# Optimization experiments

Measured on AMD Instinct MI355X. Metric: run time of the kernel, lower is better.

Reference implementation:

```python
import jax, jax.numpy as jnp
import numpy as np

N = 50000   # nodes
E = 800000  # edges
F = 128     # feat_dim
LN_EPS = 1e-5


def setup_inputs() -> dict:
    key = jax.random.key(0)
    ks = jax.random.split(key, 16)

    def lin(k, fan_in, shape):
        # roughly kaiming-uniform-like scale; exact init is irrelevant for correctness
        return jax.random.normal(k, shape, jnp.float32) * (1.0 / np.sqrt(fan_in))

    inp = {
        "x": jax.random.normal(ks[0], (N, F), jnp.float32),
        "pos": jax.random.normal(ks[1], (N, 3), jnp.float32),
        "edge_index": jax.random.randint(ks[2], (2, E), 0, N, jnp.int64),
        # edge_mlp: Linear(2F+1 -> F), SiLU, Linear(F -> F)
        "ew1": lin(ks[3], 2 * F + 1, (2 * F + 1, F)),
        "eb1": jnp.zeros((F,), jnp.float32),
        "ew2": lin(ks[4], F, (F, F)),
        "eb2": jnp.zeros((F,), jnp.float32),
        # node_mlp: Linear(F -> F), SiLU, Linear(F -> F)
        "nw1": lin(ks[5], F, (F, F)),
        "nb1": jnp.zeros((F,), jnp.float32),
        "nw2": lin(ks[6], F, (F, F)),
        "nb2": jnp.zeros((F,), jnp.float32),
        # coord_mlp: Linear(F -> 1), Tanh
        "cw": lin(ks[7], F, (F, 1)),
        "cb": jnp.zeros((1,), jnp.float32),
        # LayerNorm(F)
        "gamma": jnp.ones((F,), jnp.float32),
        "beta": jnp.zeros((F,), jnp.float32),
    }
    return inp


def reference(x, pos, edge_index, ew1, eb1, ew2, eb2, nw1, nb1, nw2, nb2, cw, cb, gamma, beta):
    row, col = edge_index[0], edge_index[1]

    diff = pos[row] - pos[col]                              # [E, 3]
    dist2 = jnp.sum(diff * diff, axis=1, keepdims=True)     # [E, 1]
    edge_feat = jnp.concatenate([x[row], x[col], dist2], axis=1)  # [E, 2F+1]

    # edge MLP (dropout p=0 -> identity in eval)
    msg = jax.nn.silu(edge_feat @ ew1 + eb1) @ ew2 + eb2    # [E, F]

    # scatter-add messages to source nodes
    agg = jax.ops.segment_sum(msg, row, num_segments=N)     # [N, F]

    # node MLP + residual + LayerNorm
    upd = jax.nn.silu(agg @ nw1 + nb1) @ nw2 + nb2          # [N, F]
    pre = x + upd
    mean = jnp.mean(pre, axis=-1, keepdims=True)
    var = jnp.mean(jnp.square(pre - mean), axis=-1, keepdims=True)
    x_out = gamma * (pre - mean) * jax.lax.rsqrt(var + LN_EPS) + beta

    # coordinate update
    scale = jnp.tanh(msg @ cw + cb)                         # [E, 1]
    delta = jax.ops.segment_sum(scale * diff, row, num_segments=N)  # [N, 3]
    pos_out = pos + delta
    return (x_out, pos_out)
```

## Files before the change

### kernel.cpp

```cpp
#include <hip/hip_runtime.h>
#include <math.h>

#define NN 50000
#define EE 800000
#define FF 128

constexpr float LN_EPS = 1e-5f;
constexpr int NC = (NN + 255) / 256;

typedef float  f32x4  __attribute__((ext_vector_type(4)));
typedef short  s16x8  __attribute__((ext_vector_type(8)));
typedef unsigned short u16x4 __attribute__((ext_vector_type(4)));

__device__ __forceinline__ float silu_f(float v) {
    return v / (1.f + __expf(-v));
}

__device__ __forceinline__ unsigned short f2bf(float f) {
    union { float f; unsigned u; } cv; cv.f = f;
    unsigned u = cv.u;
    u += 0x7fffu + ((u >> 16) & 1u);
    return (unsigned short)(u >> 16);
}

__device__ __forceinline__ float bf2f(unsigned short u) {
    union { unsigned u; float f; } cv; cv.u = ((unsigned)u) << 16;
    return cv.f;
}

constexpr int CVT_BLKS  = (NN * FF / 8) / 256;
constexpr int TRW_BLKS  = (32768 + 3 * 16384) / 256;
constexpr int HIST_BLKS = (EE + 255) / 256;

__global__ __launch_bounds__(256) void prep_kernel(
    const float* __restrict__ x, unsigned short* __restrict__ xb,
    const float* __restrict__ ew1, const float* __restrict__ ew2,
    const float* __restrict__ nw1, const float* __restrict__ nw2,
    unsigned short* __restrict__ ew1T, unsigned short* __restrict__ ew2T,
    unsigned short* __restrict__ nw1T, unsigned short* __restrict__ nw2T,
    const int* __restrict__ ei, int* __restrict__ cnt)
{
    if (blockIdx.x < CVT_BLKS) {
        int i = (blockIdx.x * 256 + threadIdx.x) * 8;
        float4 a = *(const float4*)&x[i];
        float4 b = *(const float4*)&x[i + 4];
        s16x8 o;
        o[0] = (short)f2bf(a.x); o[1] = (short)f2bf(a.y);
        o[2] = (short)f2bf(a.z); o[3] = (short)f2bf(a.w);
        o[4] = (short)f2bf(b.x); o[5] = (short)f2bf(b.y);
        o[6] = (short)f2bf(b.z); o[7] = (short)f2bf(b.w);
        *(s16x8*)&xb[i] = o;
    } else if (blockIdx.x < CVT_BLKS + TRW_BLKS) {
        int o = (blockIdx.x - CVT_BLKS) * 256 + threadIdx.x;
        if (o < 32768) {
            int n = o >> 8, k = o & 255;
            ew1T[o] = f2bf(ew1[k * FF + n]);
        } else if (o < 49152) {
            int o2 = o - 32768; int n = o2 >> 7, k = o2 & 127;
            ew2T[o2] = f2bf(ew2[k * FF + n]);
        } else if (o < 65536) {
            int o2 = o - 49152; int n = o2 >> 7, k = o2 & 127;
            nw1T[o2] = f2bf(nw1[k * FF + n]);
        } else {
            int o2 = o - 65536; int n = o2 >> 7, k = o2 & 127;
            nw2T[o2] = f2bf(nw2[k * FF + n]);
        }
    } else {
        int e = (blockIdx.x - CVT_BLKS - TRW_BLKS) * 256 + threadIdx.x;
        if (e < EE) atomicAdd(&cnt[ei[e]], 1);
    }
}

constexpr int YABS = 136;
constexpr int YNBLK = (NN + 63) / 64;

__global__ __launch_bounds__(512) void nodeY_kernel(
    const unsigned short* __restrict__ xb,
    const unsigned short* __restrict__ ew1T,
    unsigned short* __restrict__ Y)
{
    __shared__ __align__(16) unsigned short aB[64 * YABS];

    const int t   = threadIdx.x;
    const int w   = t >> 6;
    const int l   = t & 63;
    const int l15 = l & 15;
    const int q8  = l >> 4;
    const int n0  = blockIdx.x * 64;
    const int n   = w * 16 + l15;

    #pragma unroll
    for (int i = 0; i < 2; ++i) {
        int idx = (i * 512 + t) * 8;
        int e = idx >> 7, c = idx & 127;
        s16x8 v = {};
        if (n0 + e < NN) v = *(const s16x8*)(xb + (size_t)(n0 + e) * FF + c);
        *(s16x8*)(aB + e * YABS + c) = v;
    }
    __syncthreads();

    s16x8 ba[4], bb[4];
    #pragma unroll
    for (int ko = 0; ko < 4; ++ko) {
        ba[ko] = *(const s16x8*)(ew1T + (size_t)n * 256 + ko * 32 + q8 * 8);
        bb[ko] = *(const s16x8*)(ew1T + (size_t)n * 256 + 128 + ko * 32 + q8 * 8);
    }

    f32x4 acc1[4] = {}, acc2[4] = {};
    #pragma unroll
    for (int mt = 0; mt < 4; ++mt) {
        const unsigned short* ar = aB + (mt * 16 + l15) * YABS + q8 * 8;
        #pragma unroll
        for (int ko = 0; ko < 4; ++ko) {
            s16x8 a = *(const s16x8*)(ar + ko * 32);
            acc1[mt] = __builtin_amdgcn_mfma_f32_16x16x32_bf16(a, ba[ko], acc1[mt], 0, 0, 0);
            acc2[mt] = __builtin_amdgcn_mfma_f32_16x16x32_bf16(a, bb[ko], acc2[mt], 0, 0, 0);
        }
    }
    #pragma unroll
    for (int mt = 0; mt < 4; ++mt) {
        #pragma unroll
        for (int r = 0; r < 4; ++r) {
            int nn = n0 + mt * 16 + q8 * 4 + r;
            if (nn < NN) {
                Y[(size_t)nn * 256 + n]       = f2bf(acc1[mt][r]);
                Y[(size_t)nn * 256 + 128 + n] = f2bf(acc2[mt][r]);
            }
        }
    }
}

__global__ __launch_bounds__(256) void chunk_sum_kernel(
    const int* __restrict__ cnt, int* __restrict__ chunkSum)
{
    __shared__ int s[256];
    int t = threadIdx.x;
    int idx = blockIdx.x * 256 + t;
    s[t] = (idx < NN) ? cnt[idx] : 0;
    __syncthreads();
    for (int off = 128; off > 0; off >>= 1) {
        if (t < off) s[t] += s[t + off];
        __syncthreads();
    }
    if (t == 0) chunkSum[blockIdx.x] = s[0];
}

__global__ __launch_bounds__(256) void scan_chunks_kernel(
    const int* __restrict__ chunkSum, int* __restrict__ chunkOff)
{
    __shared__ int s[256];
    int t = threadIdx.x;
    int v = (t < NC) ? chunkSum[t] : 0;
    s[t] = v;
    __syncthreads();
    for (int off = 1; off < 256; off <<= 1) {
        int u = (t >= off) ? s[t - off] : 0;
        __syncthreads();
        s[t] += u;
        __syncthreads();
    }
    if (t < NC) chunkOff[t] = s[t] - v;
}

__global__ __launch_bounds__(256) void scan_kernel(
    const int* __restrict__ cnt, const int* __restrict__ chunkOff,
    int* __restrict__ offs, int* __restrict__ rowStart)
{
    __shared__ int s[256];
    int t = threadIdx.x;
    int idx = blockIdx.x * 256 + t;
    int v = (idx < NN) ? cnt[idx] : 0;
    s[t] = v;
    __syncthreads();
    for (int off = 1; off < 256; off <<= 1) {
        int u = (t >= off) ? s[t - off] : 0;
        __syncthreads();
        s[t] += u;
        __syncthreads();
    }
    if (idx < NN) {
        int st = chunkOff[blockIdx.x] + s[t] - v;
        offs[idx] = st;
        rowStart[idx] = st;
    }
}

__global__ __launch_bounds__(256) void scatter_idx_kernel(
    const int* __restrict__ ei, int* __restrict__ offs,
    int2* __restrict__ sPair)
{
    int e = blockIdx.x * 256 + threadIdx.x;
    if (e < EE) {
        int r = ei[e], c = ei[EE + e];
        int p = atomicAdd(&offs[r], 1);
        sPair[p] = make_int2(r, c);
    }
}

constexpr int EPB    = 64;
constexpr int NTILE  = EE / EPB;
constexpr int GRID_A = 2500;
constexpr int XAS    = 264;
constexpr int H1S    = 136;
constexpr int MTS    = 72;

__global__ __launch_bounds__(512, 4) void edgeA_kernel(
    const unsigned short* __restrict__ Yb, const float* __restrict__ pos,
    const int2* __restrict__ sPair,
    const float* __restrict__ ew1, const float* __restrict__ eb1,
    const unsigned short* __restrict__ ew2T, const float* __restrict__ eb2,
    const float* __restrict__ cw,  const float* __restrict__ cb,
    float* __restrict__ agg, float* __restrict__ sSg)
{
    __shared__ float dist2S[EPB];
    __shared__ int   rowS[2][EPB];
    __shared__ float sPartT[EPB][8];
    __shared__ __align__(16) unsigned short ya  [EPB * XAS];
    __shared__ __align__(16) unsigned short h1  [EPB * H1S];
    __shared__ __align__(16) unsigned short msgT[FF * MTS];

    const int t   = threadIdx.x;
    const int w   = t >> 6;
    const int l   = t & 63;
    const int l15 = l & 15;
    const int q8  = l >> 4;
    const int n   = w * 16 + l15;

    int swz;
    {
        const int qd = GRID_A >> 3, r8 = GRID_A & 7;
        int xcd = blockIdx.x & 7, p8 = blockIdx.x >> 3;
        swz = (xcd < r8 ? xcd * (qd + 1) : r8 * (qd + 1) + (xcd - r8) * qd) + p8;
    }

    s16x8 B2[4];
    #pragma unroll
    for (int ko = 0; ko < 4; ++ko)
        B2[ko] = *(const s16x8*)(ew2T + (size_t)n * 128 + ko * 32 + q8 * 8);
    const float b2   = eb2[n];
    const float cwc  = cw[n];
    const float cb0  = cb[0];

    const int c8 = (t & 15) * 8;
    const int e2 = (t >> 4) * 2;
    float w256r[8], b1r[8];
    {
        float4 wa = *(const float4*)&ew1[256 * FF + c8];
        float4 wb = *(const float4*)&ew1[256 * FF + c8 + 4];
        w256r[0]=wa.x; w256r[1]=wa.y; w256r[2]=wa.z; w256r[3]=wa.w;
        w256r[4]=wb.x; w256r[5]=wb.y; w256r[6]=wb.z; w256r[7]=wb.w;
        float4 ca = *(const float4*)&eb1[c8];
        float4 cbv = *(const float4*)&eb1[c8 + 4];
        b1r[0]=ca.x; b1r[1]=ca.y; b1r[2]=ca.z; b1r[3]=ca.w;
        b1r[4]=cbv.x; b1r[5]=cbv.y; b1r[6]=cbv.z; b1r[7]=cbv.w;
    }

    const int q    = t & 31;
    const int eB   = t >> 5;
    const int ksel = (q & 15) * 8;
    const bool useRow = (q < 16);
    const int colOff = useRow ? 0 : 128;

    int   nidx[4];
    s16x8 ag[4];
    {
        int e0 = swz * EPB;
        #pragma unroll
        for (int i = 0; i < 4; ++i) {
            int2 pr = sPair[e0 + eB + 16 * i];
            nidx[i] = useRow ? pr.x : pr.y;
        }
        #pragma unroll
        for (int i = 0; i < 4; ++i)
            ag[i] = *(const s16x8*)(Yb + (size_t)nidx[i] * 256 + colOff + ksel);
    }

    int bsel = 0;
    for (int tile = swz; tile < NTILE; tile += GRID_A) {
        const int e0 = tile * EPB;

        #pragma unroll
        for (int i = 0; i < 4; ++i)
            *(s16x8*)(ya + (eB + 16 * i) * XAS + q * 8) = ag[i];
        if (t < EPB) {
            int2 pr = sPair[e0 + t];
            int r = pr.x, c = pr.y;
            rowS[bsel][t] = r;
            float dx = pos[r*3+0] - pos[c*3+0];
            float dy = pos[r*3+1] - pos[c*3+1];
            float dz = pos[r*3+2] - pos[c*3+2];
            dist2S[t] = dx*dx + dy*dy + dz*dz;
        }
        __syncthreads();

        {
            int tn  = tile + GRID_A;
            int e0n = (tn < NTILE) ? tn * EPB : 0;
            #pragma unroll
            for (int i = 0; i < 4; ++i) {
                int2 pr = sPair[e0n + eB + 16 * i];
                nidx[i] = useRow ? pr.x : pr.y;
            }
            #pragma unroll
            for (int i = 0; i < 4; ++i)
                ag[i] = *(const s16x8*)(Yb + (size_t)nidx[i] * 256 + colOff + ksel);
        }

        #pragma unroll
        for (int s = 0; s < 2; ++s) {
            int e = e2 + s;
            s16x8 y1 = *(const s16x8*)(ya + e * XAS + c8);
            s16x8 y2 = *(const s16x8*)(ya + e * XAS + 128 + c8);
            float d2 = dist2S[e];
            s16x8 o;
            #pragma unroll
            for (int j = 0; j < 8; ++j) {
                float v = bf2f((unsigned short)y1[j]) + bf2f((unsigned short)y2[j])
                        + d2 * w256r[j] + b1r[j];
                o[j] = (short)f2bf(silu_f(v));
            }
            *(s16x8*)(h1 + e * H1S + c8) = o;
        }
        __syncthreads();

        f32x4 acc2[4] = {};
        #pragma unroll
        for (int mt = 0; mt < 4; ++mt) {
            const unsigned short* hr = h1 + (mt * 16 + l15) * H1S + q8 * 8;
            #pragma unroll
            for (int ko = 0; ko < 4; ++ko) {
                s16x8 a = *(const s16x8*)(hr + ko * 32);
                acc2[mt] = __builtin_amdgcn_mfma_f32_16x16x32_bf16(a, B2[ko], acc2[mt], 0, 0, 0);
            }
        }

        #pragma unroll
        for (int mt = 0; mt < 4; ++mt) {
            u16x4 o;
            #pragma unroll
            for (int r = 0; r < 4; ++r) {
                float m = acc2[mt][r] + b2;
                o[r] = f2bf(m);
                float p = m * cwc;
                p += __shfl_xor(p, 1);
                p += __shfl_xor(p, 2);
                p += __shfl_xor(p, 4);
                p += __shfl_xor(p, 8);
                if (l15 == 0) sPartT[mt * 16 + q8 * 4 + r][w] = p;
            }
            int b  = mt * 2 + (q8 >> 1);
            int bs = b ^ (n & 7);
            *(u16x4*)(msgT + n * MTS + bs * 8 + (q8 & 1) * 4) = o;
        }
        __syncthreads();

        {
            int e  = t >> 3;
            int ww = t & 7;
            float p = sPartT[e][ww];
            p += __shfl_xor(p, 1);
            p += __shfl_xor(p, 2);
            p += __shfl_xor(p, 4);
            if (ww == 0) sSg[e0 + e] = tanhf(p + cb0);
        }

        {
            int c    = t & 127;
            int s    = t >> 7;
            int base = s * 16;
            int b0 = (2 * s)     ^ (c & 7);
            int b1 = (2 * s + 1) ^ (c & 7);
            s16x8 v0 = *(const s16x8*)(msgT + c * MTS + b0 * 8);
            s16x8 v1 = *(const s16x8*)(msgT + c * MTS + b1 * 8);
            float a  = 0.f;
            int cur  = rowS[bsel][base];
            #pragma unroll
            for (int k = 0; k < 16; ++k) {
                int r = rowS[bsel][base + k];
                if (r != cur) {
                    atomicAdd(&agg[(size_t)cur * FF + c], a);
                    a = 0.f; cur = r;
                }
                unsigned short mv = (k < 8) ? (unsigned short)v0[k]
                                            : (unsigned short)v1[k - 8];
                a += bf2f(mv);
            }
            atomicAdd(&agg[(size_t)cur * FF + c], a);
        }
        bsel ^= 1;
    }
}

constexpr int NPB  = 64;
constexpr int ABS  = 136;
constexpr int NBLK = (NN + NPB - 1) / NPB;

__global__ __launch_bounds__(512) void nodeB_kernel(
    const float* __restrict__ x, const float* __restrict__ pos,
    const float* __restrict__ agg, const float* __restrict__ sSg,
    const int2* __restrict__ sPair, const int* __restrict__ rowStart,
    const unsigned short* __restrict__ nw1T, const float* __restrict__ nb1,
    const unsigned short* __restrict__ nw2T, const float* __restrict__ nb2,
    const float* __restrict__ gamma, const float* __restrict__ beta,
    float* __restrict__ xout, float* __restrict__ posout)
{
    __shared__ __align__(16) unsigned short aB [NPB * ABS];
    __shared__ __align__(16) unsigned short h1B[NPB * ABS];
    __shared__ float sRedS[8][NPB];
    __shared__ float sRedQ[8][NPB];

    const int t   = threadIdx.x;
    const int w   = t >> 6;
    const int l   = t & 63;
    const int l15 = l & 15;
    const int q8  = l >> 4;
    const int n0  = blockIdx.x * NPB;
    const int n   = w * 16 + l15;

    #pragma unroll
    for (int i = 0; i < 4; ++i) {
        int idx = (i * 512 + t) * 4;
        int e = idx >> 7, c = idx & 127;
        u16x4 o;
        if (n0 + e < NN) {
            float4 v = *(const float4*)&agg[(size_t)(n0 + e) * FF + c];
            o[0] = f2bf(v.x); o[1] = f2bf(v.y); o[2] = f2bf(v.z); o[3] = f2bf(v.w);
        } else {
            o[0] = 0; o[1] = 0; o[2] = 0; o[3] = 0;
        }
        *(u16x4*)(aB + e * ABS + c) = o;
    }

    {
        int e  = t >> 3;
        int ch = t & 7;
        int nn = n0 + e;
        bool ok = nn < NN;
        int p0 = ok ? rowStart[nn] : 0;
        int p1 = ok ? ((nn == NN - 1) ? EE : rowStart[nn + 1]) : 0;
        float px = ok ? pos[nn*3+0] : 0.f;
        float py = ok ? pos[nn*3+1] : 0.f;
        float pz = ok ? pos[nn*3+2] : 0.f;
        float sx = 0.f, sy = 0.f, sz = 0.f;
        for (int p = p0 + ch; p < p1; p += 8) {
            int c = sPair[p].y;
            float g = sSg[p];
            sx += g * (px - pos[c*3+0]);
            sy += g * (py - pos[c*3+1]);
            sz += g * (pz - pos[c*3+2]);
        }
        #pragma unroll
        for (int off = 1; off < 8; off <<= 1) {
            sx += __shfl_xor(sx, off);
            sy += __shfl_xor(sy, off);
            sz += __shfl_xor(sz, off);
        }
        if (ch == 0 && ok) {
            posout[nn*3+0] = px + sx;
            posout[nn*3+1] = py + sy;
            posout[nn*3+2] = pz + sz;
        }
    }
    __syncthreads();

    f32x4 acc[4] = {};
    {
        s16x8 bw[4];
        #pragma unroll
        for (int ko = 0; ko < 4; ++ko)
            bw[ko] = *(const s16x8*)(nw1T + (size_t)n * 128 + ko * 32 + q8 * 8);
        #pragma unroll
        for (int mt = 0; mt < 4; ++mt) {
            const unsigned short* ar = aB + (mt * 16 + l15) * ABS + q8 * 8;
            #pragma unroll
            for (int ko = 0; ko < 4; ++ko) {
                s16x8 a = *(const s16x8*)(ar + ko * 32);
                acc[mt] = __builtin_amdgcn_mfma_f32_16x16x32_bf16(a, bw[ko], acc[mt], 0, 0, 0);
            }
        }
    }
    {
        float bb = nb1[n];
        #pragma unroll
        for (int mt = 0; mt < 4; ++mt) {
            #pragma unroll
            for (int r = 0; r < 4; ++r) {
                int e = mt * 16 + q8 * 4 + r;
                h1B[e * ABS + n] = f2bf(silu_f(acc[mt][r] + bb));
            }
        }
    }
    __syncthreads();

    f32x4 acc2[4] = {};
    {
        s16x8 bw[4];
        #pragma unroll
        for (int ko = 0; ko < 4; ++ko)
            bw[ko] = *(const s16x8*)(nw2T + (size_t)n * 128 + ko * 32 + q8 * 8);
        #pragma unroll
        for (int mt = 0; mt < 4; ++mt) {
            const unsigned short* hr = h1B + (mt * 16 + l15) * ABS + q8 * 8;
            #pragma unroll
            for (int ko = 0; ko < 4; ++ko) {
                s16x8 a = *(const s16x8*)(hr + ko * 32);
                acc2[mt] = __builtin_amdgcn_mfma_f32_16x16x32_bf16(a, bw[ko], acc2[mt], 0, 0, 0);
            }
        }
    }

    float pre[4][4];
    {
        float bb = nb2[n];
        #pragma unroll
        for (int mt = 0; mt < 4; ++mt) {
            #pragma unroll
            for (int r = 0; r < 4; ++r) {
                int e  = mt * 16 + q8 * 4 + r;
                int nn = n0 + e;
                float xv = (nn < NN) ? x[(size_t)nn * FF + n] : 0.f;
                pre[mt][r] = xv + acc2[mt][r] + bb;
            }
        }
    }
    #pragma unroll
    for (int mt = 0; mt < 4; ++mt) {
        #pragma unroll
        for (int r = 0; r < 4; ++r) {
            float s = pre[mt][r], sq = pre[mt][r] * pre[mt][r];
            s += __shfl_xor(s, 1);  sq += __shfl_xor(sq, 1);
            s += __shfl_xor(s, 2);  sq += __shfl_xor(sq, 2);
            s += __shfl_xor(s, 4);  sq += __shfl_xor(sq, 4);
            s += __shfl_xor(s, 8);  sq += __shfl_xor(sq, 8);
            if (l15 == 0) {
                int e = mt * 16 + q8 * 4 + r;
                sRedS[w][e] = s;
                sRedQ[w][e] = sq;
            }
        }
    }
    __syncthreads();

    {
        float g = gamma[n], bt = beta[n];
        #pragma unroll
        for (int mt = 0; mt < 4; ++mt) {
            #pragma unroll
            for (int r = 0; r < 4; ++r) {
                int e  = mt * 16 + q8 * 4 + r;
                int nn = n0 + e;
                if (nn < NN) {
                    float S = 0.f, Q = 0.f;
                    #pragma unroll
                    for (int ww = 0; ww < 8; ++ww) { S += sRedS[ww][e]; Q += sRedQ[ww][e]; }
                    float mean = S * (1.f / FF);
                    float var  = Q * (1.f / FF) - mean * mean;
                    xout[(size_t)nn * FF + n] =
                        g * (pre[mt][r] - mean) * rsqrtf(var + LN_EPS) + bt;
                }
            }
        }
    }
}

extern "C" void kernel_launch(void* const* d_in, const int* in_sizes, int n_in,
                              void* d_out, int out_size, void* d_ws, size_t ws_size,
                              hipStream_t stream) {
    const float* x    = (const float*)d_in[0];
    const float* pos  = (const float*)d_in[1];
    const int*   ei   = (const int*)  d_in[2];
    const float* ew1  = (const float*)d_in[3];
    const float* eb1  = (const float*)d_in[4];
    const float* ew2  = (const float*)d_in[5];
    const float* eb2  = (const float*)d_in[6];
    const float* nw1  = (const float*)d_in[7];
    const float* nb1  = (const float*)d_in[8];
    const float* nw2  = (const float*)d_in[9];
    const float* nb2  = (const float*)d_in[10];
    const float* cw   = (const float*)d_in[11];
    const float* cb   = (const float*)d_in[12];
    const float* gam  = (const float*)d_in[13];
    const float* bet  = (const float*)d_in[14];

    float* out    = (float*)d_out;
    float* xout   = out;
    float* posout = out + (size_t)NN * FF;

    auto align256 = [](size_t v) { return (v + 255) & ~(size_t)255; };
    char* ws = (char*)d_ws;

    size_t CNT_B   = align256((size_t)NN * 4);
    size_t OFFS_B  = align256((size_t)NN * 4);
    size_t RST_B   = align256((size_t)NN * 4);
    size_t CHNK_B  = align256((size_t)NC * 4 * 2);
    size_t SPAIR_B = align256((size_t)EE * 8);
    size_t XB_B    = align256((size_t)NN * FF * 2);
    size_t EW1T_B  = align256((size_t)128 * 256 * 2);
    size_t WT_B    = align256((size_t)128 * 128 * 2);
    size_t Y_B     = align256((size_t)NN * 256 * 2);
    size_t AGG_B   = align256((size_t)NN * FF * 4);

    size_t o = 0;
    int* cnt       = (int*)(ws + o);  o += CNT_B;
    int* offs      = (int*)(ws + o);  o += OFFS_B;
    int* rowStart  = (int*)(ws + o);  o += RST_B;
    int* chunkSum  = (int*)(ws + o);
    int* chunkOff  = chunkSum + NC;   o += CHNK_B;
    int2* sPair    = (int2*)(ws + o); o += SPAIR_B;
    unsigned short* xb   = (unsigned short*)(ws + o);  o += XB_B;
    unsigned short* ew1T = (unsigned short*)(ws + o);  o += EW1T_B;
    unsigned short* ew2T = (unsigned short*)(ws + o);  o += WT_B;
    unsigned short* nw1T = (unsigned short*)(ws + o);  o += WT_B;
    unsigned short* nw2T = (unsigned short*)(ws + o);  o += WT_B;
    unsigned short* Yb   = (unsigned short*)(ws + o);  o += Y_B;
    float*          agg  = (float*)(ws + o);           o += AGG_B;
    float*          sSg  = (float*)(ws + o);

    hipMemsetAsync(cnt, 0, CNT_B, stream);
    hipMemsetAsync(agg, 0, (size_t)NN * FF * 4, stream);

    prep_kernel<<<CVT_BLKS + TRW_BLKS + HIST_BLKS, 256, 0, stream>>>(
        x, xb, ew1, ew2, nw1, nw2, ew1T, ew2T, nw1T, nw2T, ei, cnt);

    nodeY_kernel<<<YNBLK, 512, 0, stream>>>(xb, ew1T, Yb);

    chunk_sum_kernel<<<NC, 256, 0, stream>>>(cnt, chunkSum);
    scan_chunks_kernel<<<1, 256, 0, stream>>>(chunkSum, chunkOff);
    scan_kernel<<<NC, 256, 0, stream>>>(cnt, chunkOff, offs, rowStart);
    scatter_idx_kernel<<<(EE + 255) / 256, 256, 0, stream>>>(ei, offs, sPair);

    edgeA_kernel<<<GRID_A, 512, 0, stream>>>(
        Yb, pos, sPair, ew1, eb1, ew2T, eb2, cw, cb, agg, sSg);

    nodeB_kernel<<<NBLK, 512, 0, stream>>>(
        x, pos, agg, sSg, sPair, rowStart,
        nw1T, nb1, nw2T, nb2, gam, bet, xout, posout);
}
```

Measured before the change: 478.6 us.

## Gather edge features directly into registers, drop ya staging buffer and swizzle

Each thread now loads the row/col Y vectors for its own two edges straight from global memory into registers and computes dist2 itself. This removes the shared-memory staging buffer ya, the dist2S array and one __syncthreads per tile. It also drops the XOR swizzle on msgT writes and reads, which simplifies addressing but may bring back LDS bank conflicts. The gather now uses 16-byte per-thread loads with a different coalescing pattern, pos is loaded redundantly by 16 threads per edge, and the smaller LDS footprint may raise occupancy.

```diff
diff --git a/kernel.cpp b/kernel.cpp
--- a/kernel.cpp
+++ b/kernel.cpp
@@ -200,7 +200,6 @@
 constexpr int EPB    = 64;
 constexpr int NTILE  = EE / EPB;
 constexpr int GRID_A = 2500;
-constexpr int XAS    = 264;
 constexpr int H1S    = 136;
 constexpr int MTS    = 72;
 
@@ -212,10 +211,8 @@
     const float* __restrict__ cw,  const float* __restrict__ cb,
     float* __restrict__ agg, float* __restrict__ sSg)
 {
-    __shared__ float dist2S[EPB];
     __shared__ int   rowS[2][EPB];
     __shared__ float sPartT[EPB][8];
-    __shared__ __align__(16) unsigned short ya  [EPB * XAS];
     __shared__ __align__(16) unsigned short h1  [EPB * H1S];
     __shared__ __align__(16) unsigned short msgT[FF * MTS];
 
@@ -255,71 +252,60 @@
         b1r[4]=cbv.x; b1r[5]=cbv.y; b1r[6]=cbv.z; b1r[7]=cbv.w;
     }
 
-    const int q    = t & 31;
-    const int eB   = t >> 5;
-    const int ksel = (q & 15) * 8;
-    const bool useRow = (q < 16);
-    const int colOff = useRow ? 0 : 128;
-
-    int   nidx[4];
-    s16x8 ag[4];
+    int2 prA, prB;
+    s16x8 yr0, yr1, yr2, yr3;
     {
         int e0 = swz * EPB;
-        #pragma unroll
-        for (int i = 0; i < 4; ++i) {
-            int2 pr = sPair[e0 + eB + 16 * i];
-            nidx[i] = useRow ? pr.x : pr.y;
-        }
-        #pragma unroll
-        for (int i = 0; i < 4; ++i)
-            ag[i] = *(const s16x8*)(Yb + (size_t)nidx[i] * 256 + colOff + ksel);
+        prA = sPair[e0 + e2];
+        prB = sPair[e0 + e2 + 1];
+        yr0 = *(const s16x8*)(Yb + (size_t)prA.x * 256 + c8);
+        yr1 = *(const s16x8*)(Yb + (size_t)prA.y * 256 + 128 + c8);
+        yr2 = *(const s16x8*)(Yb + (size_t)prB.x * 256 + c8);
+        yr3 = *(const s16x8*)(Yb + (size_t)prB.y * 256 + 128 + c8);
     }
 
     int bsel = 0;
     for (int tile = swz; tile < NTILE; tile += GRID_A) {
         const int e0 = tile * EPB;
 
-        #pragma unroll
-        for (int i = 0; i < 4; ++i)
-            *(s16x8*)(ya + (eB + 16 * i) * XAS + q * 8) = ag[i];
-        if (t < EPB) {
-            int2 pr = sPair[e0 + t];
-            int r = pr.x, c = pr.y;
-            rowS[bsel][t] = r;
-            float dx = pos[r*3+0] - pos[c*3+0];
-            float dy = pos[r*3+1] - pos[c*3+1];
-            float dz = pos[r*3+2] - pos[c*3+2];
-            dist2S[t] = dx*dx + dy*dy + dz*dz;
-        }
-        __syncthreads();
+        if (t < EPB) rowS[bsel][t] = sPair[e0 + t].x;
+
+        float d2A, d2B;
+        {
+            float ax = pos[prA.x*3+0] - pos[prA.y*3+0];
+            float ay = pos[prA.x*3+1] - pos[prA.y*3+1];
+            float az = pos[prA.x*3+2] - pos[prA.y*3+2];
+            d2A = ax*ax + ay*ay + az*az;
+            float bx = pos[prB.x*3+0] - pos[prB.y*3+0];
+            float by = pos[prB.x*3+1] - pos[prB.y*3+1];
+            float bz = pos[prB.x*3+2] - pos[prB.y*3+2];
+            d2B = bx*bx + by*by + bz*bz;
+        }
+
+        {
+            s16x8 oA, oB;
+            #pragma unroll
+            for (int j = 0; j < 8; ++j) {
+                float vA = bf2f((unsigned short)yr0[j]) + bf2f((unsigned short)yr1[j])
+                         + d2A * w256r[j] + b1r[j];
+                oA[j] = (short)f2bf(silu_f(vA));
+                float vB = bf2f((unsigned short)yr2[j]) + bf2f((unsigned short)yr3[j])
+                         + d2B * w256r[j] + b1r[j];
+                oB[j] = (short)f2bf(silu_f(vB));
+            }
+            *(s16x8*)(h1 + e2 * H1S + c8)       = oA;
+            *(s16x8*)(h1 + (e2 + 1) * H1S + c8) = oB;
+        }
 
         {
             int tn  = tile + GRID_A;
             int e0n = (tn < NTILE) ? tn * EPB : 0;
-            #pragma unroll
-            for (int i = 0; i < 4; ++i) {
-                int2 pr = sPair[e0n + eB + 16 * i];
-                nidx[i] = useRow ? pr.x : pr.y;
-            }
-            #pragma unroll
-            for (int i = 0; i < 4; ++i)
-                ag[i] = *(const s16x8*)(Yb + (size_t)nidx[i] * 256 + colOff + ksel);
-        }
-
-        #pragma unroll
-        for (int s = 0; s < 2; ++s) {
-            int e = e2 + s;
-            s16x8 y1 = *(const s16x8*)(ya + e * XAS + c8);
-            s16x8 y2 = *(const s16x8*)(ya + e * XAS + 128 + c8);
-            float d2 = dist2S[e];
-            s16x8 o;
-            #pragma unroll
-            for (int j = 0; j < 8; ++j) {
-                float v = bf2f((unsigned short)y1[j]) + bf2f((unsigned short)y2[j])
-                        + d2 * w256r[j] + b1r[j];
-                o[j] = (short)f2bf(silu_f(v));
-            }
-            *(s16x8*)(h1 + e * H1S + c8) = o;
+            prA = sPair[e0n + e2];
+            prB = sPair[e0n + e2 + 1];
+            yr0 = *(const s16x8*)(Yb + (size_t)prA.x * 256 + c8);
+            yr1 = *(const s16x8*)(Yb + (size_t)prA.y * 256 + 128 + c8);
+            yr2 = *(const s16x8*)(Yb + (size_t)prB.x * 256 + c8);
+            yr3 = *(const s16x8*)(Yb + (size_t)prB.y * 256 + 128 + c8);
         }
         __syncthreads();
 
@@ -348,9 +334,7 @@
                 p += __shfl_xor(p, 8);
                 if (l15 == 0) sPartT[mt * 16 + q8 * 4 + r][w] = p;
             }
-            int b  = mt * 2 + (q8 >> 1);
-            int bs = b ^ (n & 7);
-            *(u16x4*)(msgT + n * MTS + bs * 8 + (q8 & 1) * 4) = o;
+            *(u16x4*)(msgT + n * MTS + mt * 16 + q8 * 4) = o;
         }
         __syncthreads();
 
@@ -368,10 +352,9 @@
             int c    = t & 127;
             int s    = t >> 7;
             int base = s * 16;
-            int b0 = (2 * s)     ^ (c & 7);
-            int b1 = (2 * s + 1) ^ (c & 7);
-            s16x8 v0 = *(const s16x8*)(msgT + c * MTS + b0 * 8);
-            s16x8 v1 = *(const s16x8*)(msgT + c * MTS + b1 * 8);
+            const unsigned short* mr = msgT + c * MTS + base;
+            s16x8 v0 = *(const s16x8*)(mr);
+            s16x8 v1 = *(const s16x8*)(mr + 8);
             float a  = 0.f;
             int cur  = rowS[bsel][base];
             #pragma unroll
```

New measurement: 448.3 us. 1.07x faster.
